# Optimization experiments

Hardware: AMD Instinct MI355X
Metric: run time of the kernel (lower is better)

## Reference

```python
import math
import jax, jax.numpy as jnp
import numpy as np

B, N1, N2 = 4, 1024, 768
DIM, H, DK = 1536, 8, 64
DV = DIM // H          # 192
NRPF = DIM // H        # 192, divisible by 6
ESM_CELL = 1280 + 256  # 1536
LN_EPS = 1e-5


def layer_norm(t, g, b):
    mu = jnp.mean(t, axis=-1, keepdims=True)
    var = jnp.mean(jnp.square(t - mu), axis=-1, keepdims=True)
    return (t - mu) * jax.lax.rsqrt(var + LN_EPS) * g + b


def positional_embed(n, feature_size):
    # Enformer-style relative positional features for distances -n+1..n-1
    distances = jnp.arange(-n + 1, n, dtype=jnp.float32)  # [2n-1]
    absd = jnp.abs(distances)[:, None]
    nb = feature_size // 6  # 3 basis fns x 2 (sym + signed)
    seq_len = float(n)
    # exponential
    max_range = math.log(seq_len) / math.log(2.0)
    half_life = 2.0 ** jnp.linspace(3.0, max_range, nb)
    f_exp = jnp.exp(-math.log(2.0) / half_life * absd)
    # central mask
    widths = 2.0 ** jnp.arange(1, nb + 1, dtype=jnp.float32) - 1.0
    f_cm = (widths[None, :] > absd).astype(jnp.float32)
    # gamma pdf
    stddev = seq_len / (2.0 * nb)
    start_mean = seq_len / nb
    mean = jnp.linspace(start_mean, seq_len, nb)
    conc = (mean / stddev) ** 2
    rate = mean / stddev ** 2
    log_p = jax.scipy.special.xlogy(conc - 1.0, absd) - rate * absd
    log_norm = jax.scipy.special.gammaln(conc) - conc * jnp.log(rate)
    prob = jnp.exp(log_p - log_norm) + 1e-8
    f_gam = prob / jnp.max(prob, axis=-1, keepdims=True)
    emb = jnp.concatenate([f_exp, f_cm, f_gam], axis=-1)
    return jnp.concatenate([emb, jnp.sign(distances)[:, None] * emb], axis=-1)  # [2n-1, feature_size]


def relative_shift(x):
    # x: [b, h, t1, 2n-1] -> [b, h, t1, n]
    b, h, t1, _ = x.shape
    x = jnp.pad(x, ((0, 0), (0, 0), (0, 0), (1, 0)))
    t2 = x.shape[-1]  # 2n
    x = x.reshape(b, h, t2, t1)[:, :, 1:, :].reshape(b, h, t1, t2 - 1)
    return x[..., : (t2 + 1) // 2]


def ffn(t, g, b, w1, b1, w2, b2):
    h = layer_norm(t, g, b)
    h = jax.nn.relu(h @ w1 + b1)
    return h @ w2 + b2


def setup_inputs() -> dict:
    key = jax.random.key(0)
    ks = jax.random.split(key, 20)
    s = 0.02
    d = {
        'x': jax.random.normal(ks[0], (B, N1, DIM), jnp.float32),
        'y0': jax.random.normal(ks[1], (B, N2, ESM_CELL), jnp.float32),
        'res_w': jax.random.normal(ks[2], (ESM_CELL, DIM)) * s,
        'lnx_g': jnp.ones((DIM,)), 'lnx_b': jnp.zeros((DIM,)),
        'lny_g': jnp.ones((DIM,)), 'lny_b': jnp.zeros((DIM,)),
        'wq': jax.random.normal(ks[3], (DIM, H * DK)) * s,
        'wk': jax.random.normal(ks[4], (DIM, H * DK)) * s,
        'wv1': jax.random.normal(ks[5], (DIM, H * DV)) * s,
        'wv2': jax.random.normal(ks[6], (DIM, H * DV)) * s,
        'wrel': jax.random.normal(ks[7], (NRPF, H * DK)) * s,
        'rel_pos_bias': jax.random.normal(ks[8], (1, H, 1, DK)),
        'wo1': jax.random.normal(ks[9], (H * DV, DIM)) * s, 'bo1': jnp.zeros((DIM,)),
        'wo2': jax.random.normal(ks[10], (H * DV, DIM)) * s, 'bo2': jnp.zeros((DIM,)),
        'fx_ln_g': jnp.ones((DIM,)), 'fx_ln_b': jnp.zeros((DIM,)),
        'fx_w1': jax.random.normal(ks[11], (DIM, 2 * DIM)) * s, 'fx_b1': jnp.zeros((2 * DIM,)),
        'fx_w2': jax.random.normal(ks[12], (2 * DIM, DIM)) * s, 'fx_b2': jnp.zeros((DIM,)),
        'fy_ln_g': jnp.ones((DIM,)), 'fy_ln_b': jnp.zeros((DIM,)),
        'fy_w1': jax.random.normal(ks[13], (DIM, 2 * DIM)) * s, 'fy_b1': jnp.zeros((2 * DIM,)),
        'fy_w2': jax.random.normal(ks[14], (2 * DIM, DIM)) * s, 'fy_b2': jnp.zeros((DIM,)),
    }
    return d


def reference(x, y0, res_w, lnx_g, lnx_b, lny_g, lny_b, wq, wk, wv1, wv2,
              wrel, rel_pos_bias, wo1, bo1, wo2, bo2,
              fx_ln_g, fx_ln_b, fx_w1, fx_b1, fx_w2, fx_b2,
              fy_ln_g, fy_ln_b, fy_w1, fy_b1, fy_w2, fy_b2):
    scale = DK ** -0.5
    y = y0 @ res_w                                   # res_proj (first layer)
    x1 = layer_norm(x, lnx_g, lnx_b)
    y1 = layer_norm(y, lny_g, lny_b)

    def heads(t, dh):  # [b, n, h*dh] -> [b, h, n, dh]
        return t.reshape(t.shape[0], t.shape[1], H, dh).transpose(0, 2, 1, 3)

    q = heads(x1 @ wq, DK) * scale                   # [b,h,n1,dk]
    k = heads(y1 @ wk, DK)                           # [b,h,n2,dk]
    v2 = heads(y1 @ wv2, DV)                         # [b,h,n2,dv]

    content = jnp.einsum('bhid,bhjd->bhij', q, k)    # [b,h,n1,n2]

    pos = positional_embed(N1, NRPF)                 # [2n1-1, nrpf]
    rel_q = (pos @ wrel).reshape(2 * N1 - 1, H, DK).transpose(1, 0, 2)  # [h,2n1-1,dk]
    rel_logits = jnp.einsum('bhjd,hnd->bhjn', k * scale + rel_pos_bias, rel_q)  # [b,h,n2,2n1-1]
    rel_logits = relative_shift(rel_logits)          # [b,h,n2,n1]
    logits = content + rel_logits.transpose(0, 1, 3, 2)

    attn = jax.nn.softmax(logits, axis=-1)           # [b,h,n1,n2]

    out1 = jnp.einsum('bhij,bhjd->bhid', attn, v2)   # [b,h,n1,dv]
    out1 = out1.transpose(0, 2, 1, 3).reshape(B, N1, H * DV)
    x2 = out1 @ wo1 + bo1

    # exchange branch: reuse attn^T on v1 from stream x
    v1 = heads(x1 @ wv1, DV)                         # [b,h,n1,dv]
    out2 = jnp.einsum('bhij,bhid->bhjd', attn, v1)   # [b,h,n2,dv]
    out2 = out2.transpose(0, 2, 1, 3).reshape(B, N2, H * DV)
    y2 = out2 @ wo2 + bo2

    x4 = x + x2
    x5 = x4 + ffn(x4, fx_ln_g, fx_ln_b, fx_w1, fx_b1, fx_w2, fx_b2)
    y4 = y + y2
    y5 = y4 + ffn(y4, fy_ln_g, fy_ln_b, fy_w1, fy_b1, fy_w2, fy_b2)
    return x5, y5
```

## Files before the change

### kernel.cpp

```cpp
#include <hip/hip_runtime.h>
#include <stdint.h>
#include <math.h>

typedef __attribute__((ext_vector_type(8))) short s8v;
typedef __attribute__((ext_vector_type(4))) short s4v;
typedef __attribute__((ext_vector_type(4))) float f4v;

#define DEV static __device__ __forceinline__

DEV short f2bf(float f) {
  uint32_t u = __builtin_bit_cast(uint32_t, f);
  u += 0x7FFFu + ((u >> 16) & 1u);
  return (short)(u >> 16);
}
DEV float bf2f(short s) {
  uint32_t u = ((uint32_t)(uint16_t)s) << 16;
  return __builtin_bit_cast(float, u);
}

#define GLD16(g, l) __builtin_amdgcn_global_load_lds( \
    (const __attribute__((address_space(1))) void*)(g), \
    (__attribute__((address_space(3))) void*)(l), 16, 0, 0)

__global__ __launch_bounds__(256) void gemm_bt(
    const short* __restrict__ A, const short* __restrict__ B,
    float* Cf, short* Cb,
    const float* __restrict__ bias, const float* resid,
    int M, int N, int K, int lda, int ldb, int ldc,
    long long sAo, long long sAi, long long sBo, long long sBi,
    long long sCo, long long sCi, float alpha, int relu)
{
  __shared__ __align__(16) short lA[128*32];
  __shared__ __align__(16) short lB[128*32];
  const int z = blockIdx.z, zo = z >> 3, zi = z & 7;
  const short* Ab = A + zo*sAo + zi*sAi;
  const short* Bb = B + zo*sBo + zi*sBi;
  const long long cOff = zo*sCo + zi*sCi;

  const int m0 = blockIdx.y*128, n0 = blockIdx.x*128;
  const int tid = threadIdx.x, lane = tid & 63, wv = tid >> 6;
  const int wm = (wv >> 1)*64, wn = (wv & 1)*64;
  const int fr = lane & 15, fq = lane >> 4;

  f4v acc[4][4] = {};

  const int rA0 = min(m0 + (tid >> 2), M - 1);
  const int rA1 = min(m0 + 64 + (tid >> 2), M - 1);
  const int rB0 = min(n0 + (tid >> 2), N - 1);
  const int rB1 = min(n0 + 64 + (tid >> 2), N - 1);
  const int pc = (tid & 3) * 8;
  const short* gA0 = Ab + (size_t)rA0*lda + pc;
  const short* gA1 = Ab + (size_t)rA1*lda + pc;
  const short* gB0 = Bb + (size_t)rB0*ldb + pc;
  const short* gB1 = Bb + (size_t)rB1*ldb + pc;
  short* dA0 = lA + (wv*64)*8;
  short* dA1 = lA + (256 + wv*64)*8;
  short* dB0 = lB + (wv*64)*8;
  short* dB1 = lB + (256 + wv*64)*8;

  for (int k0 = 0; k0 < K; k0 += 32) {
    GLD16(gA0 + k0, dA0);
    GLD16(gA1 + k0, dA1);
    GLD16(gB0 + k0, dB0);
    GLD16(gB1 + k0, dB1);
    __syncthreads();
    s8v af[4], bg[4];
#pragma unroll
    for (int i = 0; i < 4; i++) {
      af[i] = *(const s8v*)&lA[(wm + i*16 + fr)*32 + fq*8];
      bg[i] = *(const s8v*)&lB[(wn + i*16 + fr)*32 + fq*8];
    }
#pragma unroll
    for (int mi = 0; mi < 4; mi++)
#pragma unroll
      for (int ni = 0; ni < 4; ni++)
        acc[mi][ni] = __builtin_amdgcn_mfma_f32_16x16x32_bf16(af[mi], bg[ni], acc[mi][ni], 0, 0, 0);
    __syncthreads();
  }

#pragma unroll
  for (int mi = 0; mi < 4; mi++) {
    const int row = m0 + wm + mi*16 + fq*4;
#pragma unroll
    for (int ni = 0; ni < 4; ni++) {
      const int col = n0 + wn + ni*16 + fr;
      if (col >= N) continue;
      const float bv = bias ? bias[col] : 0.f;
#pragma unroll
      for (int r = 0; r < 4; r++) {
        if (row + r >= M) continue;
        float v = acc[mi][ni][r] * alpha + bv;
        const long long idx = cOff + (long long)(row + r)*ldc + col;
        if (resid) v += resid[idx];
        if (relu) v = fmaxf(v, 0.f);
        if (Cf) Cf[idx] = v;
        if (Cb) Cb[idx] = f2bf(v);
      }
    }
  }
}

__global__ __launch_bounds__(256) void pv_k(
    const short* __restrict__ attnb, const short* __restrict__ v2T, short* __restrict__ out1,
    const short* __restrict__ attnT, const short* __restrict__ v1T, short* __restrict__ out2)
{
  __shared__ __align__(16) short lA[128*32];
  __shared__ __align__(16) short lB[128*32];
  const int z = blockIdx.z, b = z >> 3, h = z & 7;
  const short* A; const short* B; short* C; int M, K, lda, m0;
  if (blockIdx.y < 8) {
    A = attnb + (size_t)z*786432; B = v2T + (size_t)z*147456;
    C = out1 + ((size_t)b*1024)*1536 + h*192;
    M = 1024; K = 768; lda = 768; m0 = blockIdx.y*128;
  } else {
    A = attnT + (size_t)z*786432; B = v1T + (size_t)z*196608;
    C = out2 + ((size_t)b*768)*1536 + h*192;
    M = 768; K = 1024; lda = 1024; m0 = (blockIdx.y - 8)*128;
  }
  const int N = 192, ldc = 1536, ldb = lda;
  const int n0 = blockIdx.x*128;
  const int tid = threadIdx.x, lane = tid & 63, wv = tid >> 6;
  const int wm = (wv >> 1)*64, wn = (wv & 1)*64;
  const int fr = lane & 15, fq = lane >> 4;

  f4v acc[4][4] = {};

  const int rA0 = m0 + (tid >> 2);
  const int rA1 = m0 + 64 + (tid >> 2);
  const int rB0 = min(n0 + (tid >> 2), N - 1);
  const int rB1 = min(n0 + 64 + (tid >> 2), N - 1);
  const int pc = (tid & 3) * 8;
  const short* gA0 = A + (size_t)rA0*lda + pc;
  const short* gA1 = A + (size_t)rA1*lda + pc;
  const short* gB0 = B + (size_t)rB0*ldb + pc;
  const short* gB1 = B + (size_t)rB1*ldb + pc;
  short* dA0 = lA + (wv*64)*8;
  short* dA1 = lA + (256 + wv*64)*8;
  short* dB0 = lB + (wv*64)*8;
  short* dB1 = lB + (256 + wv*64)*8;

  for (int k0 = 0; k0 < K; k0 += 32) {
    GLD16(gA0 + k0, dA0);
    GLD16(gA1 + k0, dA1);
    GLD16(gB0 + k0, dB0);
    GLD16(gB1 + k0, dB1);
    __syncthreads();
    s8v af[4], bg[4];
#pragma unroll
    for (int i = 0; i < 4; i++) {
      af[i] = *(const s8v*)&lA[(wm + i*16 + fr)*32 + fq*8];
      bg[i] = *(const s8v*)&lB[(wn + i*16 + fr)*32 + fq*8];
    }
#pragma unroll
    for (int mi = 0; mi < 4; mi++)
#pragma unroll
      for (int ni = 0; ni < 4; ni++)
        acc[mi][ni] = __builtin_amdgcn_mfma_f32_16x16x32_bf16(af[mi], bg[ni], acc[mi][ni], 0, 0, 0);
    __syncthreads();
  }

#pragma unroll
  for (int mi = 0; mi < 4; mi++) {
    const int row = m0 + wm + mi*16 + fq*4;
#pragma unroll
    for (int ni = 0; ni < 4; ni++) {
      const int col = n0 + wn + ni*16 + fr;
      if (col >= N) continue;
#pragma unroll
      for (int r = 0; r < 4; r++)
        C[(size_t)(row + r)*ldc + col] = f2bf(acc[mi][ni][r]);
    }
  }
}

#define ST_A(buf, ks, tt) do { const int ko = ((tt)<<6) + ((ks)<<5); \
    GLD16(gA0 + ko, ldA + ((buf)*2+(ks))*8192); \
    GLD16(gA1 + ko, ldA + ((buf)*2+(ks))*8192 + 4096); } while(0)
#define ST_B(buf, ks, tt) do { const int ko = ((tt)<<6) + ((ks)<<5); \
    GLD16(gB0 + ko, ldB + ((buf)*2+(ks))*8192); \
    GLD16(gB1 + ko, ldB + ((buf)*2+(ks))*8192 + 4096); } while(0)

#define PH256(buf, ks, mig, READB, DOWAIT, ...) do { \
    s8v av[4]; \
    const int rb = ((buf)*2+(ks))*8192; \
    _Pragma("unroll") for (int q2 = 0; q2 < 4; q2++) av[q2] = *(const s8v*)&smem[rb + aoff[(mig)*4+q2]]; \
    if (READB) { _Pragma("unroll") for (int q2 = 0; q2 < 4; q2++) bv[q2] = *(const s8v*)&smem[32768 + rb + boff[q2]]; } \
    __VA_ARGS__; \
    if (DOWAIT == 1) asm volatile("s_waitcnt vmcnt(6)" ::: "memory"); \
    if (DOWAIT == 2) asm volatile("s_waitcnt vmcnt(0)" ::: "memory"); \
    __builtin_amdgcn_s_barrier(); \
    asm volatile("s_waitcnt lgkmcnt(0)" ::: "memory"); \
    __builtin_amdgcn_s_setprio(1); \
    _Pragma("unroll") for (int q2 = 0; q2 < 4; q2++) \
      _Pragma("unroll") for (int u2 = 0; u2 < 4; u2++) \
        acc[(mig)*4+q2][u2] = __builtin_amdgcn_mfma_f32_16x16x32_bf16(av[q2], bv[u2], acc[(mig)*4+q2][u2], 0, 0, 0); \
    __builtin_amdgcn_s_setprio(0); \
  } while(0)

__global__ __launch_bounds__(512) void gemm256(
    const short* __restrict__ A0p, const short* __restrict__ B0p,
    float* C0f, short* C0b, const float* __restrict__ bias0, const float* res0,
    int nb0, int nbm0, int N0, float al0,
    const short* __restrict__ A1p, const short* __restrict__ B1p,
    float* C1f, short* C1b, const float* __restrict__ bias1, const float* res1,
    int nb01, int nbm1, int N1, float al1,
    const short* __restrict__ A2p, const short* __restrict__ B2p,
    float* C2f, short* C2b, const float* __restrict__ bias2, const float* res2,
    int nbm2, int N2, float al2,
    int K, int relu)
{
  __shared__ __align__(16) short smem[65536];
  const int total = gridDim.x;
  int bid = blockIdx.x;
  if ((total & 7) == 0) bid = (bid & 7)*(total >> 3) + (bid >> 3);
  const short* A; const short* B; float* Cf; short* Cb; const float* bias; const float* resid;
  int tile, nbm, N; float alpha;
  if (bid < nb0)       { A = A0p; B = B0p; Cf = C0f; Cb = C0b; bias = bias0; resid = res0;
                         tile = bid; nbm = nbm0; N = N0; alpha = al0; }
  else if (bid < nb01) { A = A1p; B = B1p; Cf = C1f; Cb = C1b; bias = bias1; resid = res1;
                         tile = bid - nb0; nbm = nbm1; N = N1; alpha = al1; }
  else                 { A = A2p; B = B2p; Cf = C2f; Cb = C2b; bias = bias2; resid = res2;
                         tile = bid - nb01; nbm = nbm2; N = N2; alpha = al2; }
  const int bm = tile % nbm, bn = tile / nbm;
  const int m0 = bm << 8, n0 = bn << 8;
  const int t = threadIdx.x, lane = t & 63, w = t >> 6;
  const int wm = w >> 2, wn = w & 3;
  const int fr = lane & 15, fq = lane >> 4;
  const int ntk = K >> 6;

  const int r0 = t >> 2, r1 = 128 + (t >> 2), gsw = t & 3;
  const int cs0 = (gsw ^ ((r0 >> 1) & 3)) << 3;
  const int cs1 = (gsw ^ ((r1 >> 1) & 3)) << 3;
  const short* gA0 = A + (size_t)(m0 + r0)*K + cs0;
  const short* gA1 = A + (size_t)(m0 + r1)*K + cs1;
  const short* gB0 = B + (size_t)(n0 + r0)*K + cs0;
  const short* gB1 = B + (size_t)(n0 + r1)*K + cs1;
  short* const ldA = smem + w*512;
  short* const ldB = smem + 32768 + w*512;

  int aoff[8], boff[4];
#pragma unroll
  for (int mi = 0; mi < 8; mi++) { const int r = wm*128 + mi*16 + fr; aoff[mi] = r*32 + ((fq ^ ((r >> 1) & 3)) << 3); }
#pragma unroll
  for (int ni = 0; ni < 4; ni++) { const int r = wn*64 + ni*16 + fr; boff[ni] = r*32 + ((fq ^ ((r >> 1) & 3)) << 3); }

  f4v acc[8][4] = {};
  s8v bv[4];

  ST_A(0,0,0); ST_B(0,0,0); ST_A(0,1,0); ST_B(0,1,0);
  ST_B(1,0,1); ST_A(1,0,1); ST_B(1,1,1);
  asm volatile("s_waitcnt vmcnt(6)" ::: "memory");
  __builtin_amdgcn_s_barrier();
  asm volatile("" ::: "memory");

  for (int it = 0, nit = (ntk >> 1) - 1; it < nit; ++it) {
    const int t1 = 2*it + 1, t2 = 2*it + 2, t3 = 2*it + 3;
    PH256(0,0,0, 1,0, ST_A(1,1,t1));
    PH256(0,0,1, 0,0, ST_B(0,0,t2));
    PH256(0,1,0, 1,0, ST_A(0,0,t2));
    PH256(0,1,1, 0,1, ST_B(0,1,t2));
    PH256(1,0,0, 1,0, ST_A(0,1,t2));
    PH256(1,0,1, 0,0, ST_B(1,0,t3));
    PH256(1,1,0, 1,0, ST_A(1,0,t3));
    PH256(1,1,1, 0,1, ST_B(1,1,t3));
  }
  PH256(0,0,0, 1,0, ST_A(1,1,ntk-1));
  PH256(0,0,1, 0,0, );
  PH256(0,1,0, 1,0, );
  PH256(0,1,1, 0,2, );
  PH256(1,0,0, 1,0, );
  PH256(1,0,1, 0,0, );
  PH256(1,1,0, 1,0, );
  PH256(1,1,1, 0,0, );

#pragma unroll
  for (int mi = 0; mi < 8; mi++) {
    const int row = m0 + wm*128 + mi*16 + fq*4;
#pragma unroll
    for (int ni = 0; ni < 4; ni++) {
      const int col = n0 + wn*64 + ni*16 + fr;
      const float bvv = bias ? bias[col] : 0.f;
#pragma unroll
      for (int r = 0; r < 4; r++) {
        float v = acc[mi][ni][r]*alpha + bvv;
        const size_t idx = (size_t)(row + r)*N + col;
        if (resid) v += resid[idx];
        if (relu) v = fmaxf(v, 0.f);
        if (Cf) Cf[idx] = v;
        else Cb[idx] = f2bf(v);
      }
    }
  }
}

struct WTB {
  const float* src[8]; short* dst[8];
  int R[8], C[8], start[8];
  int NT;
};

__global__ __launch_bounds__(256) void wtransN(WTB b)
{
  __shared__ float t[32][33];
  const int id = blockIdx.x;
  if (id >= b.NT) return;
  int op = 0;
#pragma unroll
  for (int o = 1; o < 8; o++) if (id >= b.start[o]) op = o;
  const int loc = id - b.start[op];
  const int Cd = b.C[op], Rd = b.R[op];
  const int ncx = Cd >> 5;
  const int cx = (loc % ncx) << 5, ry = (loc / ncx) << 5;
  const float* s = b.src[op];
  short* d = b.dst[op];
  const int tx = threadIdx.x, ty = threadIdx.y;
#pragma unroll
  for (int k = 0; k < 4; k++)
    t[ty + k*8][tx] = s[(size_t)(ry + ty + k*8)*Cd + cx + tx];
  __syncthreads();
#pragma unroll
  for (int k = 0; k < 4; k++)
    d[(size_t)(cx + ty + k*8)*Rd + ry + tx] = f2bf(t[tx][ty + k*8]);
}

__global__ __launch_bounds__(256) void btrans2(
    const short* __restrict__ v1b, short* __restrict__ v1T,
    const short* __restrict__ v2b, short* __restrict__ v2T)
{
  __shared__ short t[32][33];
  const int z = blockIdx.z, b = z >> 3, h = z & 7;
  int y = blockIdx.y;
  const short* S; short* D; int ld_;
  if (y < 32) { S = v1b + ((size_t)b*1024)*1536 + h*192; D = v1T + (size_t)z*196608; ld_ = 1024; }
  else { y -= 32; S = v2b + ((size_t)b*768)*1536 + h*192; D = v2T + (size_t)z*147456; ld_ = 768; }
  const int c0 = blockIdx.x*32, r0 = y*32;
  const int tx = threadIdx.x, ty = threadIdx.y;
#pragma unroll
  for (int k = 0; k < 4; k++)
    t[ty + k*8][tx] = S[(size_t)(r0 + ty + k*8)*1536 + c0 + tx];
  __syncthreads();
#pragma unroll
  for (int k = 0; k < 4; k++)
    D[(size_t)(c0 + ty + k*8)*ld_ + r0 + tx] = t[tx][ty + k*8];
}

__global__ __launch_bounds__(256) void conv_bf(const float* __restrict__ src,
                                               short* __restrict__ dst, long long n)
{
  const long long i = ((long long)blockIdx.x*256 + threadIdx.x)*4;
  if (i >= n) return;
  const float4 v = *(const float4*)(src + i);
  s4v o = { f2bf(v.x), f2bf(v.y), f2bf(v.z), f2bf(v.w) };
  *(s4v*)(dst + i) = o;
}

__global__ __launch_bounds__(256) void ln_k(const float* __restrict__ in,
    const float* __restrict__ gam, const float* __restrict__ bet, short* __restrict__ out)
{
  const long long row = blockIdx.x;
  const float* r = in + row*1536;
  const int tid = threadIdx.x;
  float v[6], s = 0.f, s2 = 0.f;
#pragma unroll
  for (int i = 0; i < 6; i++) { v[i] = r[tid + i*256]; s += v[i]; s2 += v[i]*v[i]; }
  for (int m = 1; m < 64; m <<= 1) { s += __shfl_xor(s, m); s2 += __shfl_xor(s2, m); }
  __shared__ float rs[4], rs2[4];
  if ((tid & 63) == 0) { rs[tid>>6] = s; rs2[tid>>6] = s2; }
  __syncthreads();
  s = rs[0]+rs[1]+rs[2]+rs[3]; s2 = rs2[0]+rs2[1]+rs2[2]+rs2[3];
  const float mu  = s * (1.f/1536.f);
  const float var = s2 * (1.f/1536.f) - mu*mu;
  const float inv = rsqrtf(var + 1e-5f);
  short* o = out + row*1536;
#pragma unroll
  for (int i = 0; i < 6; i++) { int c = tid + i*256; o[c] = f2bf((v[i]-mu)*inv*gam[c] + bet[c]); }
}

__global__ __launch_bounds__(256) void ln2_k(
    const float* __restrict__ in1, const float* __restrict__ g1, const float* __restrict__ b1,
    short* __restrict__ o1,
    const float* __restrict__ in2, const float* __restrict__ g2, const float* __restrict__ b2,
    short* __restrict__ o2)
{
  long long row = blockIdx.x;
  const float* in; const float* gam; const float* bet; short* out;
  if (row < 4096) { in = in1; gam = g1; bet = b1; out = o1; }
  else { row -= 4096; in = in2; gam = g2; bet = b2; out = o2; }
  const float* r = in + row*1536;
  const int tid = threadIdx.x;
  float v[6], s = 0.f, s2 = 0.f;
#pragma unroll
  for (int i = 0; i < 6; i++) { v[i] = r[tid + i*256]; s += v[i]; s2 += v[i]*v[i]; }
  for (int m = 1; m < 64; m <<= 1) { s += __shfl_xor(s, m); s2 += __shfl_xor(s2, m); }
  __shared__ float rs[4], rs2[4];
  if ((tid & 63) == 0) { rs[tid>>6] = s; rs2[tid>>6] = s2; }
  __syncthreads();
  s = rs[0]+rs[1]+rs[2]+rs[3]; s2 = rs2[0]+rs2[1]+rs2[2]+rs2[3];
  const float mu  = s * (1.f/1536.f);
  const float var = s2 * (1.f/1536.f) - mu*mu;
  const float inv = rsqrtf(var + 1e-5f);
  short* o = out + row*1536;
#pragma unroll
  for (int i = 0; i < 6; i++) { int c = tid + i*256; o[c] = f2bf((v[i]-mu)*inv*gam[c] + bet[c]); }
}

__global__ __launch_bounds__(64) void posemb(short* __restrict__ out)
{
  const int i = blockIdx.x;
  const int j = threadIdx.x;
  const float dist = (float)(i - 1023);
  const float absd = fabsf(dist);
  float fe = 0.f, fc = 0.f, prob = 0.f;
  if (j < 32) {
    const float hl = exp2f(3.f + 7.f*(float)j/31.f);
    fe = expf(-0.6931471805599453f/hl * absd);
    const float width = exp2f((float)(j+1)) - 1.f;
    fc = (width > absd) ? 1.f : 0.f;
    const float m = 32.f*(float)(j+1);
    const float conc = (m/16.f)*(m/16.f);
    const float rate = m/256.f;
    const float logp = (absd > 0.f ? (conc-1.f)*logf(absd) : -INFINITY) - rate*absd;
    const float logn = lgammaf(conc) - conc*logf(rate);
    prob = expf(logp - logn) + 1e-8f;
  }
  float mx = prob;
  for (int m = 1; m < 32; m <<= 1) mx = fmaxf(mx, __shfl_xor(mx, m));
  if (j < 32) {
    const float fg = prob / mx;
    const float sg = dist > 0.f ? 1.f : (dist < 0.f ? -1.f : 0.f);
    const size_t base = (size_t)i*192;
    out[base + j]       = f2bf(fe);
    out[base + 32 + j]  = f2bf(fc);
    out[base + 64 + j]  = f2bf(fg);
    out[base + 96 + j]  = f2bf(sg*fe);
    out[base + 128 + j] = f2bf(sg*fc);
    out[base + 160 + j] = f2bf(sg*fg);
  }
}

__global__ __launch_bounds__(256) void relbias_k(const float* __restrict__ rpb,
    const short* __restrict__ relq, float* __restrict__ T)
{
  const int n = blockIdx.x;
  const int tid = threadIdx.x;
  const int h = tid >> 5, l = tid & 31;
  const int d = l*2;
  float s = rpb[h*64+d]   * bf2f(relq[(size_t)n*512 + h*64 + d])
          + rpb[h*64+d+1] * bf2f(relq[(size_t)n*512 + h*64 + d+1]);
  for (int m = 1; m < 32; m <<= 1) s += __shfl_xor(s, m);
  if (l == 0) T[h*2047 + n] = s;
}

__global__ __launch_bounds__(256) void scores_k(
    const short* __restrict__ qb, const short* __restrict__ kb,
    const short* __restrict__ relq, const float* __restrict__ T,
    short* __restrict__ L)
{
  __shared__ __align__(16) short smem[21504];
  short* kt  = smem;
  short* qt  = smem + 4608;
  short* rqt = smem + 4608;
  float* P   = (float*)(smem + 4608);

  const int z = blockIdx.z, b = z >> 3, h = z & 7;
  const int j0 = blockIdx.x*64, i0 = blockIdx.y*64;
  const int tid = threadIdx.x, lane = tid & 63, wv = tid >> 6;
  const int fr = lane & 15, fq = lane >> 4;

  {
    const short* kg = kb + (size_t)(b*768  + j0)*512 + h*64;
    const short* qg = qb + (size_t)(b*1024 + i0)*512 + h*64;
    for (int c = tid; c < 512; c += 256) {
      const int r = c >> 3, ch = (c & 7)*8;
      *(s8v*)&kt[r*72 + ch] = *(const s8v*)&kg[(size_t)r*512 + ch];
      *(s8v*)&qt[r*72 + ch] = *(const s8v*)&qg[(size_t)r*512 + ch];
    }
  }
  __syncthreads();

  const int wi = (wv & 1)*32, wj = (wv >> 1)*32;
  f4v c2[2][2] = {};
#pragma unroll
  for (int ks = 0; ks < 2; ks++) {
    s8v aq[2], bk[2];
#pragma unroll
    for (int mi = 0; mi < 2; mi++) aq[mi] = *(const s8v*)&qt[(wi + mi*16 + fr)*72 + ks*32 + fq*8];
#pragma unroll
    for (int ni = 0; ni < 2; ni++) bk[ni] = *(const s8v*)&kt[(wj + ni*16 + fr)*72 + ks*32 + fq*8];
#pragma unroll
    for (int mi = 0; mi < 2; mi++)
#pragma unroll
      for (int ni = 0; ni < 2; ni++)
        c2[mi][ni] = __builtin_amdgcn_mfma_f32_16x16x32_bf16(aq[mi], bk[ni], c2[mi][ni], 0, 0, 0);
  }
  __syncthreads();

  const int nbase = 704 + i0 - j0;
  {
    const short* rg = relq + (size_t)nbase*512 + h*64;
    for (int c = tid; c < 1024; c += 256) {
      const int r = c >> 3, ch = (c & 7)*8;
      *(s8v*)&rqt[r*72 + ch] = *(const s8v*)&rg[(size_t)r*512 + ch];
    }
  }
  __syncthreads();

  const int wj2 = (wv & 1)*32, wn2 = (wv >> 1)*64;
  f4v pr[2][4] = {};
#pragma unroll
  for (int ks = 0; ks < 2; ks++) {
    s8v a2[2], b2[4];
#pragma unroll
    for (int mi = 0; mi < 2; mi++) a2[mi] = *(const s8v*)&kt[(wj2 + mi*16 + fr)*72 + ks*32 + fq*8];
#pragma unroll
    for (int ni = 0; ni < 4; ni++) b2[ni] = *(const s8v*)&rqt[(wn2 + ni*16 + fr)*72 + ks*32 + fq*8];
#pragma unroll
    for (int mi = 0; mi < 2; mi++)
#pragma unroll
      for (int ni = 0; ni < 4; ni++)
        pr[mi][ni] = __builtin_amdgcn_mfma_f32_16x16x32_bf16(a2[mi], b2[ni], pr[mi][ni], 0, 0, 0);
  }
  __syncthreads();

#pragma unroll
  for (int mi = 0; mi < 2; mi++)
#pragma unroll
    for (int ni = 0; ni < 4; ni++)
#pragma unroll
      for (int r = 0; r < 4; r++)
        P[(wj2 + mi*16 + fq*4 + r)*132 + wn2 + ni*16 + fr] = pr[mi][ni][r];
  __syncthreads();

  const float* Tt = T + h*2047 + nbase;
  short* Lb = L + ((size_t)z*1024 + i0)*768 + j0;
#pragma unroll
  for (int mi = 0; mi < 2; mi++)
#pragma unroll
    for (int ni = 0; ni < 2; ni++)
#pragma unroll
      for (int r = 0; r < 4; r++) {
        const int il = wi + mi*16 + fq*4 + r;
        const int jl = wj + ni*16 + fr;
        const int nl = 63 + il - jl;
        Lb[(size_t)il*768 + jl] = f2bf(c2[mi][ni][r] + 0.125f*P[jl*132 + nl] + Tt[nl]);
      }
}

__global__ __launch_bounds__(256) void softmax2d(const short* __restrict__ L,
    short* __restrict__ attnb, short* __restrict__ attnT)
{
  __shared__ __align__(16) short pt[32*776];
  const int ic = blockIdx.x, z = blockIdx.y;
  const int t = threadIdx.x, wv = t >> 6, lane = t & 63;
  const int rl = wv*8 + (lane >> 3);
  const int cs = (lane & 7)*96;
  const size_t rowg = ((size_t)z*1024 + ic*32 + rl)*768;

  s8v v[12];
#pragma unroll
  for (int k = 0; k < 12; k++) v[k] = *(const s8v*)&L[rowg + cs + k*8];

  float mx = -1e30f;
#pragma unroll
  for (int k = 0; k < 12; k++)
#pragma unroll
    for (int e = 0; e < 8; e++) mx = fmaxf(mx, bf2f(v[k][e]));
  mx = fmaxf(mx, __shfl_xor(mx, 1));
  mx = fmaxf(mx, __shfl_xor(mx, 2));
  mx = fmaxf(mx, __shfl_xor(mx, 4));

  float s = 0.f;
#pragma unroll
  for (int k = 0; k < 12; k++)
#pragma unroll
    for (int e = 0; e < 8; e++) s += __expf(bf2f(v[k][e]) - mx);
  s += __shfl_xor(s, 1);
  s += __shfl_xor(s, 2);
  s += __shfl_xor(s, 4);
  const float inv = 1.f / s;

  short* ab = attnb + rowg;
#pragma unroll
  for (int k = 0; k < 12; k++) {
    s8v o;
#pragma unroll
    for (int e = 0; e < 8; e++) o[e] = f2bf(__expf(bf2f(v[k][e]) - mx) * inv);
    *(s8v*)&ab[cs + k*8] = o;
    *(s8v*)&pt[rl*776 + cs + k*8] = o;
  }
  __syncthreads();

  short* aT = attnT + (size_t)z*786432 + (size_t)ic*32;
  const int i4 = (lane & 7)*4, jb = lane >> 3;
  for (int jj = 0; jj < 24; jj++) {
    const int j = wv*192 + jj*8 + jb;
    s4v o;
#pragma unroll
    for (int e = 0; e < 4; e++) o[e] = pt[(i4 + e)*776 + j];
    *(s4v*)&aT[(size_t)j*1024 + i4] = o;
  }
}

static void gemm(hipStream_t st, const short* A, const short* B, float* Cf, short* Cb,
                 const float* bias, const float* resid,
                 int M, int N, int K, int lda, int ldb, int ldc,
                 int batches = 1,
                 long long sAo = 0, long long sAi = 0, long long sBo = 0, long long sBi = 0,
                 long long sCo = 0, long long sCi = 0, float alpha = 1.f, int relu = 0)
{
  dim3 g((N + 127)/128, (M + 127)/128, batches);
  gemm_bt<<<g, dim3(256), 0, st>>>(A, B, Cf, Cb, bias, resid, M, N, K, lda, ldb, ldc,
                                   sAo, sAi, sBo, sBi, sCo, sCi, alpha, relu);
}

static void g256_3(hipStream_t st,
    const short* A0, const short* B0, float* C0f, short* C0b, const float* bias0, const float* res0,
    int M0, int N0, float al0,
    const short* A1, const short* B1, float* C1f, short* C1b, const float* bias1, const float* res1,
    int M1, int N1, float al1,
    const short* A2, const short* B2, float* C2f, short* C2b, const float* bias2, const float* res2,
    int M2, int N2, float al2,
    int K, int relu)
{
  const int nbm0 = M0 >> 8, nb0 = nbm0*(N0 >> 8);
  const int nbm1 = M1 >> 8, nb1 = nbm1*(N1 >> 8);
  const int nbm2 = M2 >> 8, nb2 = M2 ? nbm2*(N2 >> 8) : 0;
  gemm256<<<dim3(nb0 + nb1 + nb2), dim3(512), 0, st>>>(
      A0, B0, C0f, C0b, bias0, res0, nb0, nbm0, N0, al0,
      A1, B1, C1f, C1b, bias1, res1, nb0 + nb1, nbm1, N1, al1,
      A2, B2, C2f, C2b, bias2, res2, nbm2, N2, al2, K, relu);
}

static void g256(hipStream_t st,
    const short* A0, const short* B0, float* C0f, short* C0b, const float* bias0, const float* res0,
    int M0, int N0, float al0,
    const short* A1, const short* B1, float* C1f, short* C1b, const float* bias1, const float* res1,
    int M1, int N1, float al1,
    int K, int relu)
{
  g256_3(st, A0, B0, C0f, C0b, bias0, res0, M0, N0, al0,
         A1, B1, C1f, C1b, bias1, res1, M1, N1, al1,
         nullptr, nullptr, nullptr, nullptr, nullptr, nullptr, 0, 256, 1.f, K, relu);
}

extern "C" void kernel_launch(void* const* d_in, const int* in_sizes, int n_in,
                              void* d_out, int out_size, void* d_ws, size_t ws_size,
                              hipStream_t stream)
{
  (void)in_sizes; (void)n_in; (void)out_size; (void)ws_size;
  const float* x     = (const float*)d_in[0];
  const float* y0    = (const float*)d_in[1];
  const float* lnxg  = (const float*)d_in[3];
  const float* lnxb  = (const float*)d_in[4];
  const float* lnyg  = (const float*)d_in[5];
  const float* lnyb  = (const float*)d_in[6];
  const float* rpb   = (const float*)d_in[12];
  const float* bo1   = (const float*)d_in[14];
  const float* bo2   = (const float*)d_in[16];
  const float* fxg   = (const float*)d_in[17];
  const float* fxbb  = (const float*)d_in[18];
  const float* fxb1  = (const float*)d_in[20];
  const float* fxb2  = (const float*)d_in[22];
  const float* fyg   = (const float*)d_in[23];
  const float* fybb  = (const float*)d_in[24];
  const float* fyb1  = (const float*)d_in[26];
  const float* fyb2  = (const float*)d_in[28];

  char* base = (char*)d_ws;
  size_t off = 0;
  auto bump = [&](size_t b) -> char* { char* p = base + off; off += (b + 255) & ~(size_t)255; return p; };

  short* W_A  = (short*)bump(4718592);
  short* W_B  = (short*)bump(1572864);
  short* W_B2 = (short*)bump(1572864);
  short* W_C  = (short*)bump(4718592);
  short* W_D  = (short*)bump(196608);
  short* W_E  = (short*)bump(9437184);
  short* W_F  = (short*)bump(9437184);

  char*  uB = bump(12582912);
  short* x1   = (short*)uB;
  short* v1T  = (short*)uB;
  char*  uC = bump(9437184);
  short* y1   = (short*)uC;
  short* out2 = (short*)uC;
  char*  uD = bump(9437184);
  short* y0b = (short*)uD;
  short* qb  = (short*)uD;
  short* kbB = (short*)(uD + 4194304);
  short* v2T = (short*)uD;
  float* Tbl   = (float*)bump(262016);
  short* posb  = (short*)bump(786048);
  short* relqb = (short*)bump(2096128);
  char*  uG = bump(12582912);
  short* v1b  = (short*)uG;
  short* out1 = (short*)uG;
  short* x4ln = (short*)uG;
  char*  uH = bump(9437184);   short* v2b = (short*)uH;  short* y4ln = (short*)uH;
  char*  uI = bump(100663296);
  short* wv2T    = (short*)uI;
  short* logits16 = (short*)uI;
  short* attnT   = (short*)(uI + 50331648);
  short* hx      = (short*)uI;
  short* hy      = (short*)(uI + 25165824);
  short* fy1T    = (short*)(uI + 46137344);
  short* fy2T    = (short*)(uI + 55574528);
  char*  U2 = bump(50331648);
  short* attnb = (short*)U2;
  float* y4    = (float*)U2;

  float* outx = (float*)d_out;
  float* outy = (float*)d_out + 6291456;
  float* x4  = outx;
  float* y_f = outy;

  auto addop = [&](WTB& b, int i, int idx, short* dst, int R, int C) {
    b.src[i] = (const float*)d_in[idx]; b.dst[i] = dst;
    b.R[i] = R; b.C[i] = C; b.start[i] = b.NT; b.NT += (R >> 5)*(C >> 5);
  };
  auto finwtb = [&](WTB& b, int n) {
    for (int i = n; i < 8; i++) { b.start[i] = 0x7fffffff; b.src[i] = nullptr; b.dst[i] = nullptr; b.R[i] = 32; b.C[i] = 32; }
  };

  WTB b1{}; b1.NT = 0;
  addop(b1, 0, 2,  W_A,  1536, 1536);
  addop(b1, 1, 11, W_D,  192,  512);
  addop(b1, 2, 9,  W_C,  1536, 1536);
  addop(b1, 3, 10, wv2T, 1536, 1536);
  addop(b1, 4, 7,  W_B,  1536, 512);
  addop(b1, 5, 8,  W_B2, 1536, 512);
  addop(b1, 6, 19, W_E,  1536, 3072);
  addop(b1, 7, 21, W_F,  3072, 1536);
  wtransN<<<dim3(b1.NT), dim3(32,8), 0, stream>>>(b1);

  conv_bf<<<4608, 256, 0, stream>>>(y0, y0b, 4718592LL);
  posemb<<<2047, 64, 0, stream>>>(posb);
  ln_k<<<4096, 256, 0, stream>>>(x, lnxg, lnxb, x1);
  gemm(stream, posb, W_D, nullptr, relqb, nullptr, nullptr, 2047, 512, 192, 192, 192, 512);
  relbias_k<<<2047, 256, 0, stream>>>(rpb, relqb, Tbl);
  g256(stream, y0b, W_A, y_f, nullptr, nullptr, nullptr, 3072, 1536, 1.f,
       x1, W_C, nullptr, v1b, nullptr, nullptr, 4096, 1536, 1.f, 1536, 0);
  WTB b2{}; b2.NT = 0;
  addop(b2, 0, 13, W_A, 1536, 1536);
  addop(b2, 1, 15, W_C, 1536, 1536);
  finwtb(b2, 2);
  wtransN<<<dim3(b2.NT), dim3(32,8), 0, stream>>>(b2);
  ln_k<<<3072, 256, 0, stream>>>(y_f, lnyg, lnyb, y1);
  g256_3(stream, y1, wv2T, nullptr, v2b, nullptr, nullptr, 3072, 1536, 1.f,
         x1, W_B, nullptr, qb, nullptr, nullptr, 4096, 512, 0.125f,
         y1, W_B2, nullptr, kbB, nullptr, nullptr, 3072, 512, 1.f, 1536, 0);
  scores_k<<<dim3(12,16,32), 256, 0, stream>>>(qb, kbB, relqb, Tbl, logits16);
  softmax2d<<<dim3(32,32), 256, 0, stream>>>(logits16, attnb, attnT);
  btrans2<<<dim3(6,56,32), dim3(32,8), 0, stream>>>(v1b, v1T, v2b, v2T);
  pv_k<<<dim3(2,14,32), 256, 0, stream>>>(attnb, v2T, out1, attnT, v1T, out2);
  WTB b3{}; b3.NT = 0;
  addop(b3, 0, 25, fy1T, 1536, 3072);
  addop(b3, 1, 27, fy2T, 3072, 1536);
  finwtb(b3, 2);
  wtransN<<<dim3(b3.NT), dim3(32,8), 0, stream>>>(b3);
  g256(stream, out1, W_A, x4, nullptr, bo1, x, 4096, 1536, 1.f,
       out2, W_C, y4, nullptr, bo2, y_f, 3072, 1536, 1.f, 1536, 0);
  ln2_k<<<7168, 256, 0, stream>>>(x4, fxg, fxbb, x4ln, y4, fyg, fybb, y4ln);
  g256(stream, x4ln, W_E, nullptr, hx, fxb1, nullptr, 4096, 3072, 1.f,
       y4ln, fy1T, nullptr, hy, fyb1, nullptr, 3072, 3072, 1.f, 1536, 1);
  g256(stream, hx, W_F, outx, nullptr, fxb2, x4, 4096, 1536, 1.f,
       hy, fy2T, outy, nullptr, fyb2, y4, 3072, 1536, 1.f, 3072, 0);
}
```

Measured before the change: 651.7 us.

## Fuse score computation and softmax into one kernel keeping logits in LDS

Merges the scores kernel and the row softmax into a single kernel where each block owns 64 query rows of one head and loops over all 12 key tiles. The full 64x768 bf16 logit strip stays in shared memory, so the logits never round-trip through global memory, and one launch is removed. In exchange the grid shrinks from 6144 blocks to 512, and each block now uses about 142KB of LDS, which sharply cuts occupancy and serialises the key-tile loop within a block.

```diff
diff --git a/kernel.cpp b/kernel.cpp
--- a/kernel.cpp
+++ b/kernel.cpp
@@ -451,152 +451,148 @@
   if (l == 0) T[h*2047 + n] = s;
 }
 
-__global__ __launch_bounds__(256) void scores_k(
+__global__ __launch_bounds__(256) void fsm_k(
     const short* __restrict__ qb, const short* __restrict__ kb,
     const short* __restrict__ relq, const float* __restrict__ T,
-    short* __restrict__ L)
-{
-  __shared__ __align__(16) short smem[21504];
-  short* kt  = smem;
-  short* qt  = smem + 4608;
-  short* rqt = smem + 4608;
-  float* P   = (float*)(smem + 4608);
-
-  const int z = blockIdx.z, b = z >> 3, h = z & 7;
-  const int j0 = blockIdx.x*64, i0 = blockIdx.y*64;
+    short* __restrict__ attnb, short* __restrict__ attnT)
+{
+  __shared__ __align__(16) short smem[71168];
+  short* lg  = smem;
+  short* kt  = smem + 49664;
+  short* rqt = smem + 54272;
+  float* P   = (float*)(smem + 54272);
+
+  const int z = blockIdx.y, b = z >> 3, h = z & 7;
+  const int i0 = blockIdx.x*64;
   const int tid = threadIdx.x, lane = tid & 63, wv = tid >> 6;
   const int fr = lane & 15, fq = lane >> 4;
-
+  const int wi = (wv & 1)*32, wj = (wv >> 1)*32;
+  const int wj2 = (wv & 1)*32, wn2 = (wv >> 1)*64;
+
+  s8v aq[2][2];
   {
-    const short* kg = kb + (size_t)(b*768  + j0)*512 + h*64;
     const short* qg = qb + (size_t)(b*1024 + i0)*512 + h*64;
-    for (int c = tid; c < 512; c += 256) {
-      const int r = c >> 3, ch = (c & 7)*8;
-      *(s8v*)&kt[r*72 + ch] = *(const s8v*)&kg[(size_t)r*512 + ch];
-      *(s8v*)&qt[r*72 + ch] = *(const s8v*)&qg[(size_t)r*512 + ch];
+#pragma unroll
+    for (int mi = 0; mi < 2; mi++)
+#pragma unroll
+      for (int ks = 0; ks < 2; ks++)
+        aq[mi][ks] = *(const s8v*)&qg[(size_t)(wi + mi*16 + fr)*512 + ks*32 + fq*8];
+  }
+  const short* kgb = kb + (size_t)(b*768)*512 + h*64;
+  const float* Th = T + h*2047;
+
+  for (int jt = 0; jt < 12; ++jt) {
+    const int j0 = jt*64;
+    const int nbase = 704 + i0 - j0;
+    __syncthreads();
+    {
+      const short* kg = kgb + (size_t)j0*512;
+      const short* rg = relq + (size_t)nbase*512 + h*64;
+      for (int c = tid; c < 512; c += 256) {
+        const int r = c >> 3, ch = (c & 7)*8;
+        *(s8v*)&kt[r*72 + ch] = *(const s8v*)&kg[(size_t)r*512 + ch];
+      }
+      for (int c = tid; c < 1024; c += 256) {
+        const int r = c >> 3, ch = (c & 7)*8;
+        *(s8v*)&rqt[r*72 + ch] = *(const s8v*)&rg[(size_t)r*512 + ch];
+      }
     }
+    __syncthreads();
+
+    f4v c2[2][2] = {};
+#pragma unroll
+    for (int ks = 0; ks < 2; ks++) {
+      s8v bk[2];
+#pragma unroll
+      for (int ni = 0; ni < 2; ni++) bk[ni] = *(const s8v*)&kt[(wj + ni*16 + fr)*72 + ks*32 + fq*8];
+#pragma unroll
+      for (int mi = 0; mi < 2; mi++)
+#pragma unroll
+        for (int ni = 0; ni < 2; ni++)
+          c2[mi][ni] = __builtin_amdgcn_mfma_f32_16x16x32_bf16(aq[mi][ks], bk[ni], c2[mi][ni], 0, 0, 0);
+    }
+
+    f4v pr[2][4] = {};
+#pragma unroll
+    for (int ks = 0; ks < 2; ks++) {
+      s8v a2[2], b2[4];
+#pragma unroll
+      for (int mi = 0; mi < 2; mi++) a2[mi] = *(const s8v*)&kt[(wj2 + mi*16 + fr)*72 + ks*32 + fq*8];
+#pragma unroll
+      for (int ni = 0; ni < 4; ni++) b2[ni] = *(const s8v*)&rqt[(wn2 + ni*16 + fr)*72 + ks*32 + fq*8];
+#pragma unroll
+      for (int mi = 0; mi < 2; mi++)
+#pragma unroll
+        for (int ni = 0; ni < 4; ni++)
+          pr[mi][ni] = __builtin_amdgcn_mfma_f32_16x16x32_bf16(a2[mi], b2[ni], pr[mi][ni], 0, 0, 0);
+    }
+    __syncthreads();
+
+#pragma unroll
+    for (int mi = 0; mi < 2; mi++)
+#pragma unroll
+      for (int ni = 0; ni < 4; ni++)
+#pragma unroll
+        for (int r = 0; r < 4; r++)
+          P[(wj2 + mi*16 + fq*4 + r)*132 + wn2 + ni*16 + fr] = pr[mi][ni][r];
+    __syncthreads();
+
+    const float* Tt = Th + nbase;
+#pragma unroll
+    for (int mi = 0; mi < 2; mi++)
+#pragma unroll
+      for (int ni = 0; ni < 2; ni++)
+#pragma unroll
+        for (int r = 0; r < 4; r++) {
+          const int il = wi + mi*16 + fq*4 + r;
+          const int jl = wj + ni*16 + fr;
+          const int nl = 63 + il - jl;
+          lg[il*776 + j0 + jl] = f2bf(c2[mi][ni][r] + 0.125f*P[jl*132 + nl] + Tt[nl]);
+        }
   }
   __syncthreads();
 
-  const int wi = (wv & 1)*32, wj = (wv >> 1)*32;
-  f4v c2[2][2] = {};
-#pragma unroll
-  for (int ks = 0; ks < 2; ks++) {
-    s8v aq[2], bk[2];
-#pragma unroll
-    for (int mi = 0; mi < 2; mi++) aq[mi] = *(const s8v*)&qt[(wi + mi*16 + fr)*72 + ks*32 + fq*8];
-#pragma unroll
-    for (int ni = 0; ni < 2; ni++) bk[ni] = *(const s8v*)&kt[(wj + ni*16 + fr)*72 + ks*32 + fq*8];
-#pragma unroll
-    for (int mi = 0; mi < 2; mi++)
-#pragma unroll
-      for (int ni = 0; ni < 2; ni++)
-        c2[mi][ni] = __builtin_amdgcn_mfma_f32_16x16x32_bf16(aq[mi], bk[ni], c2[mi][ni], 0, 0, 0);
-  }
-  __syncthreads();
-
-  const int nbase = 704 + i0 - j0;
-  {
-    const short* rg = relq + (size_t)nbase*512 + h*64;
-    for (int c = tid; c < 1024; c += 256) {
-      const int r = c >> 3, ch = (c & 7)*8;
-      *(s8v*)&rqt[r*72 + ch] = *(const s8v*)&rg[(size_t)r*512 + ch];
-    }
-  }
-  __syncthreads();
-
-  const int wj2 = (wv & 1)*32, wn2 = (wv >> 1)*64;
-  f4v pr[2][4] = {};
-#pragma unroll
-  for (int ks = 0; ks < 2; ks++) {
-    s8v a2[2], b2[4];
-#pragma unroll
-    for (int mi = 0; mi < 2; mi++) a2[mi] = *(const s8v*)&kt[(wj2 + mi*16 + fr)*72 + ks*32 + fq*8];
-#pragma unroll
-    for (int ni = 0; ni < 4; ni++) b2[ni] = *(const s8v*)&rqt[(wn2 + ni*16 + fr)*72 + ks*32 + fq*8];
-#pragma unroll
-    for (int mi = 0; mi < 2; mi++)
-#pragma unroll
-      for (int ni = 0; ni < 4; ni++)
-        pr[mi][ni] = __builtin_amdgcn_mfma_f32_16x16x32_bf16(a2[mi], b2[ni], pr[mi][ni], 0, 0, 0);
-  }
-  __syncthreads();
-
-#pragma unroll
-  for (int mi = 0; mi < 2; mi++)
-#pragma unroll
-    for (int ni = 0; ni < 4; ni++)
-#pragma unroll
-      for (int r = 0; r < 4; r++)
-        P[(wj2 + mi*16 + fq*4 + r)*132 + wn2 + ni*16 + fr] = pr[mi][ni][r];
-  __syncthreads();
-
-  const float* Tt = T + h*2047 + nbase;
-  short* Lb = L + ((size_t)z*1024 + i0)*768 + j0;
-#pragma unroll
-  for (int mi = 0; mi < 2; mi++)
-#pragma unroll
-    for (int ni = 0; ni < 2; ni++)
-#pragma unroll
-      for (int r = 0; r < 4; r++) {
-        const int il = wi + mi*16 + fq*4 + r;
-        const int jl = wj + ni*16 + fr;
-        const int nl = 63 + il - jl;
-        Lb[(size_t)il*768 + jl] = f2bf(c2[mi][ni][r] + 0.125f*P[jl*132 + nl] + Tt[nl]);
-      }
-}
-
-__global__ __launch_bounds__(256) void softmax2d(const short* __restrict__ L,
-    short* __restrict__ attnb, short* __restrict__ attnT)
-{
-  __shared__ __align__(16) short pt[32*776];
-  const int ic = blockIdx.x, z = blockIdx.y;
-  const int t = threadIdx.x, wv = t >> 6, lane = t & 63;
-  const int rl = wv*8 + (lane >> 3);
-  const int cs = (lane & 7)*96;
-  const size_t rowg = ((size_t)z*1024 + ic*32 + rl)*768;
-
-  s8v v[12];
-#pragma unroll
-  for (int k = 0; k < 12; k++) v[k] = *(const s8v*)&L[rowg + cs + k*8];
-
+  const int rr = tid >> 2, qq = tid & 3;
+  short* lr = lg + rr*776 + qq*192;
   float mx = -1e30f;
-#pragma unroll
-  for (int k = 0; k < 12; k++)
-#pragma unroll
-    for (int e = 0; e < 8; e++) mx = fmaxf(mx, bf2f(v[k][e]));
+  for (int k = 0; k < 24; k++) {
+    const int kk = ((k + qq*6) % 24)*8;
+    const s8v v = *(const s8v*)&lr[kk];
+#pragma unroll
+    for (int e = 0; e < 8; e++) mx = fmaxf(mx, bf2f(v[e]));
+  }
   mx = fmaxf(mx, __shfl_xor(mx, 1));
   mx = fmaxf(mx, __shfl_xor(mx, 2));
-  mx = fmaxf(mx, __shfl_xor(mx, 4));
-
   float s = 0.f;
-#pragma unroll
-  for (int k = 0; k < 12; k++)
-#pragma unroll
-    for (int e = 0; e < 8; e++) s += __expf(bf2f(v[k][e]) - mx);
+  for (int k = 0; k < 24; k++) {
+    const int kk = ((k + qq*6) % 24)*8;
+    const s8v v = *(const s8v*)&lr[kk];
+#pragma unroll
+    for (int e = 0; e < 8; e++) s += __expf(bf2f(v[e]) - mx);
+  }
   s += __shfl_xor(s, 1);
   s += __shfl_xor(s, 2);
-  s += __shfl_xor(s, 4);
   const float inv = 1.f / s;
 
-  short* ab = attnb + rowg;
-#pragma unroll
-  for (int k = 0; k < 12; k++) {
+  short* ab = attnb + ((size_t)z*1024 + i0 + rr)*768 + qq*192;
+  for (int k = 0; k < 24; k++) {
+    const int kk = ((k + qq*6) % 24)*8;
+    const s8v v = *(const s8v*)&lr[kk];
     s8v o;
 #pragma unroll
-    for (int e = 0; e < 8; e++) o[e] = f2bf(__expf(bf2f(v[k][e]) - mx) * inv);
-    *(s8v*)&ab[cs + k*8] = o;
-    *(s8v*)&pt[rl*776 + cs + k*8] = o;
+    for (int e = 0; e < 8; e++) o[e] = f2bf(__expf(bf2f(v[e]) - mx) * inv);
+    *(s8v*)&ab[kk] = o;
+    *(s8v*)&lr[kk] = o;
   }
   __syncthreads();
 
-  short* aT = attnT + (size_t)z*786432 + (size_t)ic*32;
-  const int i4 = (lane & 7)*4, jb = lane >> 3;
-  for (int jj = 0; jj < 24; jj++) {
-    const int j = wv*192 + jj*8 + jb;
+  short* aT = attnT + (size_t)z*786432 + (size_t)i0;
+  const int i4 = (lane & 15)*4, jb = lane >> 4;
+  for (int jj = 0; jj < 48; jj++) {
+    const int j = wv*192 + jj*4 + jb;
     s4v o;
 #pragma unroll
-    for (int e = 0; e < 4; e++) o[e] = pt[(i4 + e)*776 + j];
+    for (int e = 0; e < 4; e++) o[e] = lg[(i4 + e)*776 + j];
     *(s4v*)&aT[(size_t)j*1024 + i4] = o;
   }
 }
@@ -699,7 +695,6 @@
   char*  uH = bump(9437184);   short* v2b = (short*)uH;  short* y4ln = (short*)uH;
   char*  uI = bump(100663296);
   short* wv2T    = (short*)uI;
-  short* logits16 = (short*)uI;
   short* attnT   = (short*)(uI + 50331648);
   short* hx      = (short*)uI;
   short* hy      = (short*)(uI + 25165824);
@@ -749,8 +744,7 @@
   g256_3(stream, y1, wv2T, nullptr, v2b, nullptr, nullptr, 3072, 1536, 1.f,
          x1, W_B, nullptr, qb, nullptr, nullptr, 4096, 512, 0.125f,
          y1, W_B2, nullptr, kbB, nullptr, nullptr, 3072, 512, 1.f, 1536, 0);
-  scores_k<<<dim3(12,16,32), 256, 0, stream>>>(qb, kbB, relqb, Tbl, logits16);
-  softmax2d<<<dim3(32,32), 256, 0, stream>>>(logits16, attnb, attnT);
+  fsm_k<<<dim3(16,32), 256, 0, stream>>>(qb, kbB, relqb, Tbl, attnb, attnT);
   btrans2<<<dim3(6,56,32), dim3(32,8), 0, stream>>>(v1b, v1T, v2b, v2T);
   pv_k<<<dim3(2,14,32), 256, 0, stream>>>(attnb, v2T, out1, attnT, v1T, out2);
   WTB b3{}; b3.NT = 0;
```

Measured after the change: 678.7 us. 1.04x slower.
